# Performance work log

Hardware: AMD Instinct MI355X
Metric: run time of the kernel (lower is better)

The kernel has to match this reference:

```python
import jax, jax.numpy as jnp
import numpy as np

T, B, N = 1000, 64, 512
DT = 0.01
EL, VR, TR, TINF = -0.07, -0.07, -0.06, -0.05
A_VAL = 2.6239240169525146
A1_VAL = -0.015625353902578354
A2_VAL = -1.0590057373046875
B_VAL = 12.77495288848877
G_VAL = 45.24007797241211
K1, K2 = 200.0, 20.0
R1, R2 = 0.3858567178249359, -1.1421641111373901
C = 1.0


def setup_inputs() -> dict:
    key = jax.random.key(0)
    x = jax.random.normal(key, (T, B, N), dtype=jnp.float32)
    linear = jnp.ones((1, N), jnp.float32)
    a = jnp.full((1, N), A_VAL, jnp.float32)
    A1 = jnp.full((1, N), A1_VAL * C, jnp.float32)
    A2 = jnp.full((1, N), A2_VAL * C, jnp.float32)
    return {"x": x, "linear": linear, "a": a, "A1": A1, "A2": A2}


def _spike(v):
    # Heaviside step (forward of SurrGradSpike)
    return (v > 0).astype(v.dtype)


def reference(x, linear, a, A1, A2):
    G = G_VAL * C

    def step(state, xt):
        V, i1, i2, Thr = state
        i1 = i1 - K1 * i1 * DT
        i2 = i2 - K2 * i2 * DT
        V = V + DT * (linear * xt + i1 + i2 - G * (V - EL)) / C
        Thr = Thr + DT * (a * (V - EL) - B_VAL * (Thr - TINF))
        spk = _spike(V - Thr)
        i1 = (1.0 - spk) * i1 + spk * (R1 * i1 + A1)
        i2 = (1.0 - spk) * i2 + spk * (R2 * i2 + A2)
        Thr = (1.0 - spk) * Thr + spk * jnp.maximum(Thr, TR)
        V = (1.0 - spk) * V + spk * VR
        return (V, i1, i2, Thr), spk

    Bd, Nd = x.shape[1], x.shape[2]
    init = (
        jnp.full((Bd, Nd), EL, x.dtype),   # V
        jnp.zeros((Bd, Nd), x.dtype),      # i1
        jnp.zeros((Bd, Nd), x.dtype),      # i2
        jnp.full((Bd, Nd), TINF, x.dtype), # Thr
    )
    _, spikes = jax.lax.scan(step, init, x)
    return spikes  # [T, B, N] (original returns np.array of per-step spikes)
```

## Files before the change

### kernel.cpp

```cpp
#include <hip/hip_runtime.h>


#define T_STEPS 1000
#define B_DIM 64
#define N_DIM 512
#define BN (B_DIM * N_DIM)

#define K_CHUNK 20
#define NCHUNK (T_STEPS / K_CHUNK)

#define C_DT   0.01f
#define C_EL   (-0.07f)
#define C_VR   (-0.07f)
#define C_TR   (-0.06f)
#define C_TINF (-0.05f)
#define C_B    12.77495288848877f
#define C_G    45.24007797241211f
#define C_K1   200.0f
#define C_K2   20.0f
#define C_R1   0.3858567178249359f
#define C_R2   (-1.1421641111373901f)

typedef const __attribute__((address_space(1))) void* gp_t;
typedef __attribute__((address_space(3))) void* lp_t;

__device__ __forceinline__ void raw_barrier() {
    asm volatile("s_barrier" ::: "memory");
}

__device__ __forceinline__ float mn_step(float xt, float lin, float av,
                                         float A1v, float A2v,
                                         float& V, float& i1, float& i2,
                                         float& Thr)
{
#pragma clang fp contract(off)
    i1 = i1 - (C_K1 * i1) * C_DT;
    i2 = i2 - (C_K2 * i2) * C_DT;
    float p  = lin * xt;
    float q  = p + i1;
    float r  = q + i2;
    float e  = V - C_EL;
    float g  = C_G * e;
    float s  = r - g;
    float d  = C_DT * s;
    V = V + d;
    float e2 = V - C_EL;
    float u  = av * e2;
    float w  = Thr - C_TINF;
    float bw = C_B * w;
    float s2 = u - bw;
    float d2 = C_DT * s2;
    Thr = Thr + d2;
    float diff = V - Thr;
    bool  sb   = diff > 0.0f;
    float spk  = sb ? 1.0f : 0.0f;
    float i1r = (C_R1 * i1) + A1v;
    float i2r = (C_R2 * i2) + A2v;
    i1  = sb ? i1r : i1;
    i2  = sb ? i2r : i2;
    float tm = fmaxf(Thr, C_TR);
    Thr = sb ? tm : Thr;
    V   = sb ? C_VR : V;
    return spk;
}

__global__ __launch_bounds__(128) void mn_neuron_kernel(
    const float* __restrict__ x, const float* __restrict__ linear,
    const float* __restrict__ a, const float* __restrict__ A1,
    const float* __restrict__ A2, float* __restrict__ out)
{
#pragma clang fp contract(off)
    __shared__ float lds[2][K_CHUNK][64];

    const int lane = threadIdx.x & 63;
    const int wid  = threadIdx.x >> 6;
    const int blk  = blockIdx.x;

    if (wid == 1) {
        const float* pl = x + (size_t)(lane >> 4) * BN
                            + (size_t)blk * 64 + (size_t)(lane & 15) * 4;

        {
#pragma unroll
            for (int s = 0; s < K_CHUNK / 4; ++s) {
                __builtin_amdgcn_global_load_lds(
                    (gp_t)(pl + (size_t)(s * 4) * BN),
                    (lp_t)&lds[0][s * 4][0], 16, 0, 0);
            }
            asm volatile("s_waitcnt vmcnt(0)" ::: "memory");
        }
        raw_barrier();

        for (int c = 0; c < NCHUNK; ++c) {
            if (c + 1 < NCHUNK) {
                const float* pc = pl + (size_t)((c + 1) * K_CHUNK) * BN;
                float* dst = &lds[(c + 1) & 1][0][0];
#pragma unroll
                for (int s = 0; s < K_CHUNK / 4; ++s) {
                    __builtin_amdgcn_global_load_lds(
                        (gp_t)(pc + (size_t)(s * 4) * BN),
                        (lp_t)(dst + s * 4 * 64), 16, 0, 0);
                }
                asm volatile("s_waitcnt vmcnt(0)" ::: "memory");
            }
            raw_barrier();
        }
    } else {
        const int idx = blk * 64 + lane;
        const int n   = idx & (N_DIM - 1);

        const float lin = linear[n];
        const float av  = a[n];
        const float A1v = A1[n];
        const float A2v = A2[n];

        float V   = C_EL;
        float i1  = 0.0f;
        float i2  = 0.0f;
        float Thr = C_TINF;

        float* op = out + idx;

        raw_barrier();

        for (int c = 0; c < NCHUNK; ++c) {
            const float* src = &lds[c & 1][0][lane];

            float xv[K_CHUNK];
#pragma unroll
            for (int j = 0; j < K_CHUNK; ++j)
                xv[j] = src[j * 64];

#pragma unroll
            for (int j = 0; j < K_CHUNK; ++j) {
                float spk = mn_step(xv[j], lin, av, A1v, A2v, V, i1, i2, Thr);
                __builtin_nontemporal_store(spk, op);
                op += BN;
            }
            raw_barrier();
        }
    }
}

extern "C" void kernel_launch(void* const* d_in, const int* in_sizes, int n_in,
                              void* d_out, int out_size, void* d_ws, size_t ws_size,
                              hipStream_t stream) {
    const float* x      = (const float*)d_in[0];
    const float* linear = (const float*)d_in[1];
    const float* a      = (const float*)d_in[2];
    const float* A1     = (const float*)d_in[3];
    const float* A2     = (const float*)d_in[4];
    float* out = (float*)d_out;

    mn_neuron_kernel<<<BN / 64, 128, 0, stream>>>(x, linear, a, A1, A2, out);
}
```

Before: 234.4 us.

## Deepen LDS prefetch pipeline to four buffers with partial vmcnt waits

The producer wave now keeps up to three chunks of x in flight in a four-slot LDS ring, waiting only for the oldest chunk with partial vmcnt counts instead of draining all loads each iteration. This is meant to hide global-load latency behind the compute wave's recurrence. The compute wave also forces all LDS reads into registers before the step loop via empty asm constraints, so the LDS reads are not interleaved with the serial dependency chain. The cost is more LDS per block, which may lower occupancy, and barrier counts that must stay exactly matched between the two waves.

```diff
diff --git a/kernel.cpp b/kernel.cpp
--- a/kernel.cpp
+++ b/kernel.cpp
@@ -8,6 +8,7 @@
 
 #define K_CHUNK 20
 #define NCHUNK (T_STEPS / K_CHUNK)
+#define NBUF 4
 
 #define C_DT   0.01f
 #define C_EL   (-0.07f)
@@ -70,7 +71,7 @@
     const float* __restrict__ A2, float* __restrict__ out)
 {
 #pragma clang fp contract(off)
-    __shared__ float lds[2][K_CHUNK][64];
+    __shared__ float lds[NBUF][K_CHUNK][64];
 
     const int lane = threadIdx.x & 63;
     const int wid  = threadIdx.x >> 6;
@@ -80,31 +81,31 @@
         const float* pl = x + (size_t)(lane >> 4) * BN
                             + (size_t)blk * 64 + (size_t)(lane & 15) * 4;
 
-        {
+        auto issue = [&](int k) {
+            const float* pc = pl + (size_t)(k * K_CHUNK) * BN;
+            float* dst = &lds[k & (NBUF - 1)][0][0];
 #pragma unroll
             for (int s = 0; s < K_CHUNK / 4; ++s) {
                 __builtin_amdgcn_global_load_lds(
-                    (gp_t)(pl + (size_t)(s * 4) * BN),
-                    (lp_t)&lds[0][s * 4][0], 16, 0, 0);
+                    (gp_t)(pc + (size_t)(s * 4) * BN),
+                    (lp_t)(dst + s * 4 * 64), 16, 0, 0);
             }
-            asm volatile("s_waitcnt vmcnt(0)" ::: "memory");
-        }
+        };
+
+        issue(0); issue(1); issue(2);
+        asm volatile("s_waitcnt vmcnt(10)" ::: "memory");
         raw_barrier();
 
-        for (int c = 0; c < NCHUNK; ++c) {
-            if (c + 1 < NCHUNK) {
-                const float* pc = pl + (size_t)((c + 1) * K_CHUNK) * BN;
-                float* dst = &lds[(c + 1) & 1][0][0];
-#pragma unroll
-                for (int s = 0; s < K_CHUNK / 4; ++s) {
-                    __builtin_amdgcn_global_load_lds(
-                        (gp_t)(pc + (size_t)(s * 4) * BN),
-                        (lp_t)(dst + s * 4 * 64), 16, 0, 0);
-                }
-                asm volatile("s_waitcnt vmcnt(0)" ::: "memory");
-            }
+        for (int c = 0; c < NCHUNK - 3; ++c) {
+            issue(c + 3);
+            asm volatile("s_waitcnt vmcnt(10)" ::: "memory");
             raw_barrier();
         }
+        asm volatile("s_waitcnt vmcnt(5)" ::: "memory");
+        raw_barrier();
+        asm volatile("s_waitcnt vmcnt(0)" ::: "memory");
+        raw_barrier();
+        raw_barrier();
     } else {
         const int idx = blk * 64 + lane;
         const int n   = idx & (N_DIM - 1);
@@ -124,12 +125,15 @@
         raw_barrier();
 
         for (int c = 0; c < NCHUNK; ++c) {
-            const float* src = &lds[c & 1][0][lane];
+            const float* src = &lds[c & (NBUF - 1)][0][lane];
 
             float xv[K_CHUNK];
 #pragma unroll
             for (int j = 0; j < K_CHUNK; ++j)
                 xv[j] = src[j * 64];
+#pragma unroll
+            for (int j = 0; j < K_CHUNK; ++j)
+                asm volatile("" : "+v"(xv[j]));
 
 #pragma unroll
             for (int j = 0; j < K_CHUNK; ++j) {
```

Measured after the change: 236.5 us. Within noise of the previous version (+0.9%).

## Stage spike outputs in LDS and offload vectorized stores to producer wave

Applied to the files above, without the earlier changes.

The compute wave now writes spikes into a double-buffered LDS staging area instead of issuing per-element global stores. The producer wave drains the previous chunk with 16-byte nontemporal vector stores while prefetching the next input chunk. Constants are pinned in scalar registers through an asm barrier, and the compute wave raises its priority. This takes global store traffic off the serial recurrence path, at the cost of extra LDS traffic and a wider wait on each barrier.

```diff
diff --git a/kernel.cpp b/kernel.cpp
--- a/kernel.cpp
+++ b/kernel.cpp
@@ -9,58 +9,51 @@
 #define K_CHUNK 20
 #define NCHUNK (T_STEPS / K_CHUNK)
 
-#define C_DT   0.01f
-#define C_EL   (-0.07f)
-#define C_VR   (-0.07f)
-#define C_TR   (-0.06f)
-#define C_TINF (-0.05f)
-#define C_B    12.77495288848877f
-#define C_G    45.24007797241211f
-#define C_K1   200.0f
-#define C_K2   20.0f
-#define C_R1   0.3858567178249359f
-#define C_R2   (-1.1421641111373901f)
-
 typedef const __attribute__((address_space(1))) void* gp_t;
 typedef __attribute__((address_space(3))) void* lp_t;
+typedef float f32x4 __attribute__((ext_vector_type(4)));
 
 __device__ __forceinline__ void raw_barrier() {
     asm volatile("s_barrier" ::: "memory");
 }
 
+struct Consts {
+    float k200, k20, kDT, kEL, kG, kTINF, kB, kR1, kR2, kTR;
+};
+
 __device__ __forceinline__ float mn_step(float xt, float lin, float av,
-                                         float A1v, float A2v,
+                                         float A1v, float A2v, const Consts& K,
                                          float& V, float& i1, float& i2,
                                          float& Thr)
 {
 #pragma clang fp contract(off)
-    i1 = i1 - (C_K1 * i1) * C_DT;
-    i2 = i2 - (C_K2 * i2) * C_DT;
+    i1 = i1 - (K.k200 * i1) * K.kDT;
+    i2 = i2 - (K.k20  * i2) * K.kDT;
     float p  = lin * xt;
     float q  = p + i1;
     float r  = q + i2;
-    float e  = V - C_EL;
-    float g  = C_G * e;
+    float e  = V - K.kEL;
+    float g  = K.kG * e;
     float s  = r - g;
-    float d  = C_DT * s;
+    float d  = K.kDT * s;
     V = V + d;
-    float e2 = V - C_EL;
+    float e2 = V - K.kEL;
     float u  = av * e2;
-    float w  = Thr - C_TINF;
-    float bw = C_B * w;
+    float w  = Thr - K.kTINF;
+    float bw = K.kB * w;
     float s2 = u - bw;
-    float d2 = C_DT * s2;
+    float d2 = K.kDT * s2;
     Thr = Thr + d2;
     float diff = V - Thr;
     bool  sb   = diff > 0.0f;
     float spk  = sb ? 1.0f : 0.0f;
-    float i1r = (C_R1 * i1) + A1v;
-    float i2r = (C_R2 * i2) + A2v;
+    float i1r = (K.kR1 * i1) + A1v;
+    float i2r = (K.kR2 * i2) + A2v;
     i1  = sb ? i1r : i1;
     i2  = sb ? i2r : i2;
-    float tm = fmaxf(Thr, C_TR);
+    float tm = fmaxf(Thr, K.kTR);
     Thr = sb ? tm : Thr;
-    V   = sb ? C_VR : V;
+    V   = sb ? K.kEL : V;
     return spk;
 }
 
@@ -70,7 +63,8 @@
     const float* __restrict__ A2, float* __restrict__ out)
 {
 #pragma clang fp contract(off)
-    __shared__ float lds[2][K_CHUNK][64];
+    __shared__ float xb_buf[2][K_CHUNK][64];
+    __shared__ float sb_buf[2][K_CHUNK][64];
 
     const int lane = threadIdx.x & 63;
     const int wid  = threadIdx.x >> 6;
@@ -79,32 +73,45 @@
     if (wid == 1) {
         const float* pl = x + (size_t)(lane >> 4) * BN
                             + (size_t)blk * 64 + (size_t)(lane & 15) * 4;
+        float* outp = out + (size_t)blk * 64;
 
-        {
+        auto issue = [&](int k) {
+            const float* pc = pl + (size_t)(k * K_CHUNK) * BN;
+            float* dst = &xb_buf[k & 1][0][0];
 #pragma unroll
-            for (int s = 0; s < K_CHUNK / 4; ++s) {
+            for (int s5 = 0; s5 < K_CHUNK / 4; ++s5) {
                 __builtin_amdgcn_global_load_lds(
-                    (gp_t)(pl + (size_t)(s * 4) * BN),
-                    (lp_t)&lds[0][s * 4][0], 16, 0, 0);
+                    (gp_t)(pc + (size_t)(s5 * 4) * BN),
+                    (lp_t)(dst + s5 * 4 * 64), 16, 0, 0);
             }
-            asm volatile("s_waitcnt vmcnt(0)" ::: "memory");
-        }
+        };
+
+        const int r0 = lane >> 4;
+        const int c4 = (lane & 15) * 4;
+        auto flush = [&](int k) {
+            const int kb = k & 1;
+#pragma unroll
+            for (int pz = 0; pz < K_CHUNK / 4; ++pz) {
+                const int row = pz * 4 + r0;
+                const f32x4 v = *reinterpret_cast<const f32x4*>(
+                    &sb_buf[kb][row][c4]);
+                f32x4* dp = reinterpret_cast<f32x4*>(
+                    outp + (size_t)(k * K_CHUNK + row) * BN + c4);
+                __builtin_nontemporal_store(v, dp);
+            }
+        };
+
+        issue(0);
+        asm volatile("s_waitcnt vmcnt(0)" ::: "memory");
         raw_barrier();
 
         for (int c = 0; c < NCHUNK; ++c) {
-            if (c + 1 < NCHUNK) {
-                const float* pc = pl + (size_t)((c + 1) * K_CHUNK) * BN;
-                float* dst = &lds[(c + 1) & 1][0][0];
-#pragma unroll
-                for (int s = 0; s < K_CHUNK / 4; ++s) {
-                    __builtin_amdgcn_global_load_lds(
-                        (gp_t)(pc + (size_t)(s * 4) * BN),
-                        (lp_t)(dst + s * 4 * 64), 16, 0, 0);
-                }
-                asm volatile("s_waitcnt vmcnt(0)" ::: "memory");
-            }
+            if (c + 1 < NCHUNK) issue(c + 1);
+            if (c >= 1)         flush(c - 1);
+            asm volatile("s_waitcnt vmcnt(0) lgkmcnt(0)" ::: "memory");
             raw_barrier();
         }
+        flush(NCHUNK - 1);
     } else {
         const int idx = blk * 64 + lane;
         const int n   = idx & (N_DIM - 1);
@@ -114,29 +121,31 @@
         const float A1v = A1[n];
         const float A2v = A2[n];
 
-        float V   = C_EL;
+        Consts K = {200.0f, 20.0f, 0.01f, -0.07f,
+                    45.24007797241211f, -0.05f, 12.77495288848877f,
+                    0.3858567178249359f, -1.1421641111373901f, -0.06f};
+        asm volatile("" : "+s"(K.k200), "+s"(K.k20), "+s"(K.kDT),
+                          "+s"(K.kEL), "+s"(K.kG), "+s"(K.kTINF),
+                          "+s"(K.kB), "+s"(K.kR1), "+s"(K.kR2), "+s"(K.kTR));
+
+        float V   = K.kEL;
         float i1  = 0.0f;
         float i2  = 0.0f;
-        float Thr = C_TINF;
+        float Thr = K.kTINF;
 
-        float* op = out + idx;
-
+        asm volatile("s_setprio 1" ::: "memory");
         raw_barrier();
 
         for (int c = 0; c < NCHUNK; ++c) {
-            const float* src = &lds[c & 1][0][lane];
-
-            float xv[K_CHUNK];
-#pragma unroll
-            for (int j = 0; j < K_CHUNK; ++j)
-                xv[j] = src[j * 64];
-
+            const float* src = &xb_buf[c & 1][0][lane];
+            float*       dst = &sb_buf[c & 1][0][lane];
 #pragma unroll
             for (int j = 0; j < K_CHUNK; ++j) {
-                float spk = mn_step(xv[j], lin, av, A1v, A2v, V, i1, i2, Thr);
-                __builtin_nontemporal_store(spk, op);
-                op += BN;
+                float xt  = src[j * 64];
+                float spk = mn_step(xt, lin, av, A1v, A2v, K, V, i1, i2, Thr);
+                dst[j * 64] = spk;
             }
+            asm volatile("s_waitcnt lgkmcnt(0)" ::: "memory");
             raw_barrier();
         }
     }
```

Measured after the change: 232.1 us. No clear change (-1.0%).
